# Kernel tuning notes

Hardware: AMD Instinct MI355X
Metric: run time of the kernel (lower is better)

Reference implementation:

```python
import jax, jax.numpy as jnp
import numpy as np

K = 11  # masked conv3d kernel size

def mask_A(k):
    # mask type 'A': flattened (i,j,t) positions with current_id < k^3//2 + 1
    # (current_id starts at 1) -> first k^3//2 positions are 1.
    m = (np.arange(k ** 3) < (k ** 3) // 2).astype(np.float32).reshape(k, k, k)
    return jnp.asarray(m)

def conv3d(x, w, b, pad):
    out = jax.lax.conv_general_dilated(
        x, w, window_strides=(1, 1, 1), padding=[(pad, pad)] * 3,
        dimension_numbers=('NCDHW', 'OIDHW', 'NCDHW'))
    return out + b[None, :, None, None, None]

def conv2d(x, w, b, pad):
    out = jax.lax.conv_general_dilated(
        x, w, window_strides=(1, 1), padding=[(pad, pad)] * 2,
        dimension_numbers=('NCHW', 'OIHW', 'NCHW'))
    return out + b[None, :, None, None]

def pconv(x, w, b):
    # 1x1x1 conv3d as channel GEMM; w: [O, C]
    return jnp.einsum('bcdhw,oc->bodhw', x, w) + b[None, :, None, None, None]

def _phi(z):
    return 0.5 * (1.0 + jax.lax.erf(z / jnp.sqrt(2.0).astype(z.dtype)))

def setup_inputs() -> dict:
    key = jax.random.key(0)
    ks = jax.random.split(key, 12)
    M = 192
    B, H, W = 1, 48, 48
    s = 0.02
    x = jax.random.normal(ks[0], (B, M, H, W), jnp.float32)
    hyper = jax.random.normal(ks[1], (B, 2 * M, H, W), jnp.float32)
    W3 = s * jax.random.normal(ks[2], (M, 2 * M, 3, 3), jnp.float32)
    b3 = jnp.zeros((M,), jnp.float32)
    W1 = s * jax.random.normal(ks[3], (24, 1, K, K, K), jnp.float32)
    b1 = jnp.zeros((24,), jnp.float32)
    Wa = s * jax.random.normal(ks[4], (48, 25), jnp.float32)
    ba = jnp.zeros((48,), jnp.float32)
    Wb = s * jax.random.normal(ks[5], (96, 48), jnp.float32)
    bb = jnp.zeros((96,), jnp.float32)
    Wc = s * jax.random.normal(ks[6], (9, 96), jnp.float32)
    bc = jnp.zeros((9,), jnp.float32)
    return {"x": x, "hyper": hyper, "W3": W3, "b3": b3, "W1": W1, "b1": b1,
            "Wa": Wa, "ba": ba, "Wb": Wb, "bb": bb, "Wc": Wc, "bc": bc}

def reference(x, hyper, W3, b3, W1, b1, Wa, ba, Wb, bb, Wc, bc):
    # x: [B,M,H,W], hyper: [B,2M,H,W]
    x5 = x[:, None]                                   # [B,1,M,H,W]
    h = conv2d(hyper, W3, b3, 1)[:, None]             # [B,1,M,H,W]
    W1m = W1 * mask_A(K)[None, None]                  # causal mask re-applied each fwd
    x1 = conv3d(x5, W1m, b1, 5)                       # [B,24,M,H,W]
    t = jnp.concatenate([x1, h], axis=1)              # [B,25,M,H,W]
    t = jax.nn.relu(pconv(t, Wa, ba))                 # [B,48,M,H,W]
    t = jax.nn.relu(pconv(t, Wb, bb))                 # [B,96,M,H,W]
    out = pconv(t, Wc, bc)                            # [B,9,M,H,W]
    # 3-component weighted Gaussian entropy model
    mu = out[:, 0:3]
    sc = out[:, 3:6]
    sc = jnp.abs(jnp.where(sc == 0.0, 1e-9, sc))
    w = jax.nn.softmax(out[:, 6:9], axis=1)
    xe = x[:, None]                                   # [B,1,M,H,W]
    lik = jnp.abs(_phi((xe + 0.5 - mu) / sc) - _phi((xe - 0.5 - mu) / sc))
    p3 = jnp.sum(w * lik, axis=1)                     # [B,M,H,W]
    return (p3, out)
```

## Files before the change

kernel.cpp:

```cpp
#include <hip/hip_runtime.h>
#include <hip/hip_fp16.h>
#include <math.h>

#define HW    2304
#define NPOS  442368

typedef _Float16 f16x8 __attribute__((ext_vector_type(8)));
typedef __fp16   h16x2 __attribute__((ext_vector_type(2)));
typedef float    f32x4 __attribute__((ext_vector_type(4)));

__device__ __forceinline__ float phi_f(float z) {
    return 0.5f * (1.0f + erff(z * 0.70710678118654752f));
}
__device__ __forceinline__ unsigned short f2h(float v) {
    _Float16 h = (_Float16)v;
    return *reinterpret_cast<unsigned short*>(&h);
}
__device__ __forceinline__ unsigned int pk2(float a, float b) {
    return (unsigned int)f2h(a) | ((unsigned int)f2h(b) << 16);
}
__device__ __forceinline__ unsigned int pkrtz(float a, float b) {
    h16x2 h = __builtin_amdgcn_cvt_pkrtz(a, b);
    return *reinterpret_cast<unsigned int*>(&h);
}

__global__ __launch_bounds__(256) void prep_all(const float* __restrict__ hyper,
                                                const float* __restrict__ W3,
                                                const float* __restrict__ W1,
                                                const float* __restrict__ Wa,
                                                const float* __restrict__ ba,
                                                const float* __restrict__ b1,
                                                const float* __restrict__ Wb,
                                                const float* __restrict__ bb,
                                                const float* __restrict__ Wc,
                                                const float* __restrict__ xg,
                                                unsigned short* __restrict__ hyperTp,
                                                unsigned short* __restrict__ apack,
                                                unsigned short* __restrict__ pk,
                                                unsigned short* __restrict__ xhp) {
    const int bx = blockIdx.x;
    if (bx < 948) {
        __shared__ float s[32][33];
        const int pt = bx % 79, it = bx / 79;
        const int tid = threadIdx.x;
        const int c = tid & 31, r = tid >> 5;
        const int pp = pt * 32 + c;
        const int yp = pp / 50, xp = pp % 50;
        const bool inter = (pp < 2500) && yp >= 1 && yp <= 48 && xp >= 1 && xp <= 48;
        const int src = inter ? ((yp - 1) * 48 + (xp - 1)) : 0;
#pragma unroll
        for (int i = 0; i < 4; ++i) {
            int icl = r + i * 8;
            s[icl][c] = inter ? hyper[(size_t)(it * 32 + icl) * HW + src] : 0.f;
        }
        __syncthreads();
#pragma unroll
        for (int i = 0; i < 4; ++i) {
            int pl = r + i * 8;
            int pp2 = pt * 32 + pl;
            if (pp2 < 2500)
                hyperTp[(size_t)pp2 * 384 + it * 32 + c] = f2h(s[c][pl]);
        }
    } else if (bx < 3540) {
        int idx = (bx - 948) * 256 + threadIdx.x;
        int j = idx & 7;
        int l = (idx >> 3) & 63;
        int rest = idx >> 9;
        int t = rest % 9; rest /= 9;
        int c = rest % 12; int T = rest / 12;
        int oc = T * 16 + (l & 15);
        int ic = c * 32 + (l >> 4) * 8 + j;
        apack[idx] = f2h(W3[((size_t)oc * 384 + ic) * 9 + t]);
    } else if (bx < 3700) {
        int idx = (bx - 3540) * 256 + threadIdx.x;
        if (idx >= 40960) return;
        float v = 0.f;
        if (idx < 31744) {
            int j = idx & 7, lane = (idx >> 3) & 63, s = (idx >> 9) & 1, c = idx >> 10;
            int q = lane >> 4;
            int oc = s * 16 + (lane & 15);
            int r = 2 * c + (q >> 1), h = q & 1, kw = 8 * h + j;
            if (oc < 24 && r < 61 && kw < 11) {
                int kd = r / 11, kh = r % 11;
                int tap = kd * 121 + kh * 11 + kw;
                if (tap < 665) v = W1[oc * 1331 + tap];
            }
        } else if (idx < 33280) {
            int i2 = idx - 31744;
            int j = i2 & 7, lane = (i2 >> 3) & 63, t = i2 >> 9;
            int m = t * 16 + (lane & 15), k = (lane >> 4) * 8 + j;
            if (k < 25) v = Wa[m * 25 + k];
            else if (k == 25) {
                float s = ba[m];
                for (int c = 0; c < 24; ++c) s += Wa[m * 25 + c] * b1[c];
                v = s;
            }
        } else if (idx < 39424) {
            int i3 = idx - 33280;
            int j = i3 & 7, lane = (i3 >> 3) & 63, k2 = (i3 >> 9) & 1, s = i3 >> 10;
            int m = s * 16 + (lane & 15), ch = k2 * 32 + (lane >> 4) * 8 + j;
            if (ch < 48) v = Wb[m * 48 + ch];
            else if (ch == 48) v = bb[m];
        } else {
            int i4 = idx - 39424;
            int j = i4 & 7, lane = (i4 >> 3) & 63, k3 = i4 >> 9;
            int m = lane & 15, ch = k3 * 32 + (lane >> 4) * 8 + j;
            if (m < 9) v = Wc[m * 96 + ch];
        }
        pk[idx] = f2h(v);
    } else {
        int idx = (bx - 3700) * 256 + threadIdx.x;
        if (idx >= 187456) return;
        int si = idx * 4;
        int zp = si / 3712, rem = si - zp * 3712;
        int yp = rem >> 6, xp0 = rem & 63;
        float f[4];
#pragma unroll
        for (int k = 0; k < 4; ++k) {
            int xp = xp0 + k;
            bool in = zp >= 5 && zp < 197 && yp >= 5 && yp < 53 && xp >= 5 && xp < 53;
            f[k] = in ? xg[(size_t)(zp - 5) * HW + (yp - 5) * 48 + (xp - 5)] : 0.f;
        }
        *(uint2*)&xhp[si] = make_uint2(pk2(f[0], f[1]), pk2(f[2], f[3]));
    }
}

__global__ __launch_bounds__(256) void fused3(const unsigned short* __restrict__ xhp,
                                              const unsigned short* __restrict__ pk,
                                              const unsigned short* __restrict__ hyperTp,
                                              const unsigned short* __restrict__ apack,
                                              const float* __restrict__ b3,
                                              const float* __restrict__ xg,
                                              const float* __restrict__ bc,
                                              float* __restrict__ out) {
    __shared__ __align__(16) unsigned short P[6656];
    __shared__ __align__(16) unsigned short t1s[4][1152];
    __shared__ __align__(16) unsigned short t2s[4][1664];
    __shared__ __align__(16) float fscr[3328];
    __shared__ __align__(16) float htile[256];

    const int tid = threadIdx.x, w = tid >> 6, lane = tid & 63;
    const int n = lane & 15, q = lane >> 4;
    const int bx = blockIdx.x;
    const int x0 = (bx % 12) * 4, y0 = ((bx / 12) % 12) * 4;
    const int T = bx / 144, d0 = T * 16;

#pragma unroll
    for (int k = 0; k < 3; ++k) {
        int idx = tid + k * 256;
        if (idx < 588) {
            int row = idx >> 1, half = idx & 1;
            int py = row / 21, pz = row - py * 21;
            const uint4* src = (const uint4*)(xhp + ((size_t)(d0 + pz) * 58 + (y0 + py)) * 64
                                              + x0 + half * 8);
            *(uint4*)&P[row * 16 + half * 8] = *src;
        }
    }

    {
        f32x4 hacc = {0.f, 0.f, 0.f, 0.f};
        const int pp = (y0 + (n >> 2)) * 50 + x0 + (n & 3);
        const size_t bbase = (size_t)pp * 384 + q * 8;
        for (int cc = 0; cc < 3; ++cc) {
            const int c = w * 3 + cc;
            const unsigned short* ap = apack + ((size_t)(T * 12 + c) * 9) * 512 + lane * 8;
            const int coff = c * 32;
#pragma unroll
            for (int t = 0; t < 9; ++t) {
                f16x8 a = *(const f16x8*)(ap + t * 512);
                const int dd = (t / 3) * 50 + (t % 3);
                f16x8 b = *(const f16x8*)(hyperTp + bbase + (size_t)dd * 384 + coff);
                hacc = __builtin_amdgcn_mfma_f32_16x16x32_f16(a, b, hacc, 0, 0, 0);
            }
        }
#pragma unroll
        for (int e = 0; e < 4; ++e)
            fscr[w * 256 + (q * 4 + e) * 16 + n] = hacc[e];
    }
    __syncthreads();

    {
        const int oc = tid >> 4, pos = tid & 15;
        float h = b3[d0 + oc];
#pragma unroll
        for (int ww = 0; ww < 4; ++ww) h += fscr[ww * 256 + oc * 16 + pos];
        htile[oc * 16 + pos] = h;
    }

    const f32x4 zf = {0.f, 0.f, 0.f, 0.f};
    f32x4 acc[4][2];
#pragma unroll
    for (int p = 0; p < 4; ++p) { acc[p][0] = zf; acc[p][1] = zf; }

    const f16x8* Av = (const f16x8*)pk;
    f16x8 a0 = Av[lane], a1 = Av[64 + lane];
    unsigned int u[6];
    {
        const int r0 = (q >> 1);
        const int kd = r0 / 11, kh = r0 - kd * 11;
        const unsigned short* rp = P + ((w + kh) * 21 + (n + kd)) * 16 + (q & 1) * 8;
        *(uint4*)&u[0] = *(const uint4*)rp;
        *(uint2*)&u[4] = *(const uint2*)(rp + 8);
    }
    for (int c = 0; c < 31; ++c) {
        unsigned int u2[6];
        {
            const int r = 2 * (c + 1) + (q >> 1);
            const int kd = r / 11, kh = r - kd * 11;
            const unsigned short* rp = P + ((w + kh) * 21 + (n + kd)) * 16 + (q & 1) * 8;
            *(uint4*)&u2[0] = *(const uint4*)rp;
            *(uint2*)&u2[4] = *(const uint2*)(rp + 8);
        }
        f16x8 ca0 = a0, ca1 = a1;
        const int cn = (c < 30) ? c + 1 : 30;
        a0 = Av[cn * 128 + lane];
        a1 = Av[cn * 128 + 64 + lane];
#pragma unroll
        for (int px = 0; px < 4; ++px) {
            unsigned int bw[4];
#pragma unroll
            for (int i = 0; i < 4; ++i) {
                if ((px & 1) == 0) bw[i] = u[(px >> 1) + i];
                else bw[i] = (u[(px >> 1) + i] >> 16) | (u[(px >> 1) + 1 + i] << 16);
            }
            f16x8 bf = *(f16x8*)bw;
            acc[px][0] = __builtin_amdgcn_mfma_f32_16x16x32_f16(ca0, bf, acc[px][0], 0, 0, 0);
            acc[px][1] = __builtin_amdgcn_mfma_f32_16x16x32_f16(ca1, bf, acc[px][1], 0, 0, 0);
        }
#pragma unroll
        for (int i = 0; i < 6; ++i) u[i] = u2[i];
    }
    __syncthreads();

#pragma unroll
    for (int px = 0; px < 4; ++px) {
        unsigned int lo = pk2(acc[px][0][0], acc[px][0][1]);
        unsigned int hi = pk2(acc[px][0][2], acc[px][0][3]);
        *(uint2*)&P[(w * 16 + n) * 104 + px * 24 + q * 4] = make_uint2(lo, hi);
        if (q < 2) {
            unsigned int l2 = pk2(acc[px][1][0], acc[px][1][1]);
            unsigned int h2 = pk2(acc[px][1][2], acc[px][1][3]);
            *(uint2*)&P[(w * 16 + n) * 104 + px * 24 + 16 + q * 4] = make_uint2(l2, h2);
        }
    }

    const volatile f16x8* WaF = (const volatile f16x8*)(pk + 31744);
    const volatile f16x8* WbF = (const volatile f16x8*)(pk + 33280);
    const volatile f16x8* WcF = (const volatile f16x8*)(pk + 39424);
    float bcv[4];
#pragma unroll
    for (int e = 0; e < 4; ++e) bcv[e] = (q * 4 + e < 9) ? bc[q * 4 + e] : 0.f;
    *(uint2*)&t1s[w][n * 72 + 48 + q * 4] = make_uint2((q == 0) ? 0x00003C00u : 0u, 0u);

    const f16x8 z8 = {};
    for (int px = 0; px < 4; ++px) {
        f16x8 b0;
        if (q < 3) {
            b0 = *(const f16x8*)&P[(w * 16 + n) * 104 + px * 24 + q * 8];
        } else {
            b0 = z8;
            b0[0] = (_Float16)htile[n * 16 + w * 4 + px];
            b0[1] = (_Float16)1.0f;
        }
#pragma unroll
        for (int s = 0; s < 3; ++s) {
            f16x8 a = WaF[s * 64 + lane];
            f32x4 r1 = __builtin_amdgcn_mfma_f32_16x16x32_f16(a, b0, zf, 0, 0, 0);
            *(uint2*)&t1s[w][n * 72 + s * 16 + q * 4] =
                make_uint2(pkrtz(fmaxf(r1[0], 0.f), fmaxf(r1[1], 0.f)),
                           pkrtz(fmaxf(r1[2], 0.f), fmaxf(r1[3], 0.f)));
        }
        f32x4 rb[6];
#pragma unroll
        for (int s = 0; s < 6; ++s) rb[s] = zf;
#pragma unroll
        for (int k2 = 0; k2 < 2; ++k2) {
            f16x8 bf = *(const f16x8*)&t1s[w][n * 72 + k2 * 32 + q * 8];
#pragma unroll
            for (int s = 0; s < 6; ++s) {
                f16x8 a = WbF[(s * 2 + k2) * 64 + lane];
                rb[s] = __builtin_amdgcn_mfma_f32_16x16x32_f16(a, bf, rb[s], 0, 0, 0);
            }
        }
#pragma unroll
        for (int s = 0; s < 6; ++s)
            *(uint2*)&t2s[w][n * 104 + s * 16 + q * 4] =
                make_uint2(pkrtz(fmaxf(rb[s][0], 0.f), fmaxf(rb[s][1], 0.f)),
                           pkrtz(fmaxf(rb[s][2], 0.f), fmaxf(rb[s][3], 0.f)));
        f32x4 rc = zf;
#pragma unroll
        for (int k3 = 0; k3 < 3; ++k3) {
            f16x8 bf = *(const f16x8*)&t2s[w][n * 104 + k3 * 32 + q * 8];
            f16x8 a = WcF[k3 * 64 + lane];
            rc = __builtin_amdgcn_mfma_f32_16x16x32_f16(a, bf, rc, 0, 0, 0);
        }
#pragma unroll
        for (int e = 0; e < 4; ++e) {
            const int row = q * 4 + e;
            if (row < 9) fscr[w * 832 + (n * 4 + px) * 13 + row] = rc[e] + bcv[e];
        }
    }

    {
        float o[9];
#pragma unroll
        for (int jj = 0; jj < 9; ++jj) o[jj] = fscr[w * 832 + lane * 13 + jj];
        const int gp = (d0 + (lane >> 2)) * HW + (y0 + w) * 48 + x0 + (lane & 3);
        const float xv = xg[gp];
        float m = fmaxf(o[6], fmaxf(o[7], o[8]));
        float e0 = expf(o[6] - m), e1 = expf(o[7] - m), e2 = expf(o[8] - m);
        float inv_es = 1.0f / (e0 + e1 + e2);
        float p = 0.f;
#pragma unroll
        for (int jj = 0; jj < 3; ++jj) {
            float mu = o[jj];
            float sc = o[3 + jj];
            sc = (sc == 0.0f) ? 1e-9f : sc;
            sc = fabsf(sc);
            float a = phi_f((xv + 0.5f - mu) / sc);
            float b = phi_f((xv - 0.5f - mu) / sc);
            float lik = fabsf(a - b);
            float wgt = ((jj == 0) ? e0 : (jj == 1) ? e1 : e2) * inv_es;
            p = fmaf(wgt, lik, p);
        }
        out[gp] = p;
#pragma unroll
        for (int jj = 0; jj < 9; ++jj) out[NPOS + (size_t)jj * NPOS + gp] = o[jj];
    }
}

extern "C" void kernel_launch(void* const* d_in, const int* in_sizes, int n_in,
                              void* d_out, int out_size, void* d_ws, size_t ws_size,
                              hipStream_t stream) {
    const float* x     = (const float*)d_in[0];
    const float* hyper = (const float*)d_in[1];
    const float* W3    = (const float*)d_in[2];
    const float* b3    = (const float*)d_in[3];
    const float* W1    = (const float*)d_in[4];
    const float* b1    = (const float*)d_in[5];
    const float* Wa    = (const float*)d_in[6];
    const float* ba    = (const float*)d_in[7];
    const float* Wb    = (const float*)d_in[8];
    const float* bb    = (const float*)d_in[9];
    const float* Wc    = (const float*)d_in[10];
    const float* bc    = (const float*)d_in[11];
    float* out = (float*)d_out;

    unsigned short* hyperTp = (unsigned short*)d_ws;
    unsigned short* apack   = hyperTp + 960000;
    unsigned short* pk      = apack + 663552;
    unsigned short* xhp     = pk + 40960;

    prep_all<<<4433, 256, 0, stream>>>(hyper, W3, W1, Wa, ba, b1, Wb, bb, Wc, x,
                                       hyperTp, apack, pk, xhp);
    fused3<<<1728, 256, 0, stream>>>(xhp, pk, hyperTp, apack, b3, x, bc, out);
}
```

Baseline: 182.5 us.

## Shrink fused3 LDS via buffer aliasing, hoist MLP weights, fully unroll conv loop

Merges the t1s, t2s and fscr shared buffers into one aliased region and reuses P for the final 9-channel outputs, which cuts LDS per block so more blocks can be resident. It sets launch_bounds(256,4) to target higher occupancy. The MLP weights are preloaded into registers instead of being reloaded through volatile pointers, and the 31-step masked conv loop is fully unrolled with compile-time offsets in place of the manual double-buffered prefetch. The risks are register pressure from the hoisted weights under the occupancy bound, and lost load/MFMA overlap if the compiler schedules the unrolled loop poorly.

```diff
diff --git a/kernel.cpp b/kernel.cpp
--- a/kernel.cpp
+++ b/kernel.cpp
@@ -125,18 +125,16 @@
     }
 }
 
-__global__ __launch_bounds__(256) void fused3(const unsigned short* __restrict__ xhp,
-                                              const unsigned short* __restrict__ pk,
-                                              const unsigned short* __restrict__ hyperTp,
-                                              const unsigned short* __restrict__ apack,
-                                              const float* __restrict__ b3,
-                                              const float* __restrict__ xg,
-                                              const float* __restrict__ bc,
-                                              float* __restrict__ out) {
+__global__ __launch_bounds__(256, 4) void fused3(const unsigned short* __restrict__ xhp,
+                                                 const unsigned short* __restrict__ pk,
+                                                 const unsigned short* __restrict__ hyperTp,
+                                                 const unsigned short* __restrict__ apack,
+                                                 const float* __restrict__ b3,
+                                                 const float* __restrict__ xg,
+                                                 const float* __restrict__ bc,
+                                                 float* __restrict__ out) {
     __shared__ __align__(16) unsigned short P[6656];
-    __shared__ __align__(16) unsigned short t1s[4][1152];
-    __shared__ __align__(16) unsigned short t2s[4][1664];
-    __shared__ __align__(16) float fscr[3328];
+    __shared__ __align__(16) unsigned short U[11264];
     __shared__ __align__(16) float htile[256];
 
     const int tid = threadIdx.x, w = tid >> 6, lane = tid & 63;
@@ -144,6 +142,8 @@
     const int bx = blockIdx.x;
     const int x0 = (bx % 12) * 4, y0 = ((bx / 12) % 12) * 4;
     const int T = bx / 144, d0 = T * 16;
+
+    float* hpart = (float*)U;
 
 #pragma unroll
     for (int k = 0; k < 3; ++k) {
@@ -161,6 +161,7 @@
         f32x4 hacc = {0.f, 0.f, 0.f, 0.f};
         const int pp = (y0 + (n >> 2)) * 50 + x0 + (n & 3);
         const size_t bbase = (size_t)pp * 384 + q * 8;
+#pragma unroll
         for (int cc = 0; cc < 3; ++cc) {
             const int c = w * 3 + cc;
             const unsigned short* ap = apack + ((size_t)(T * 12 + c) * 9) * 512 + lane * 8;
@@ -175,7 +176,7 @@
         }
 #pragma unroll
         for (int e = 0; e < 4; ++e)
-            fscr[w * 256 + (q * 4 + e) * 16 + n] = hacc[e];
+            hpart[w * 256 + (q * 4 + e) * 16 + n] = hacc[e];
     }
     __syncthreads();
 
@@ -183,7 +184,7 @@
         const int oc = tid >> 4, pos = tid & 15;
         float h = b3[d0 + oc];
 #pragma unroll
-        for (int ww = 0; ww < 4; ++ww) h += fscr[ww * 256 + oc * 16 + pos];
+        for (int ww = 0; ww < 4; ++ww) h += hpart[ww * 256 + oc * 16 + pos];
         htile[oc * 16 + pos] = h;
     }
 
@@ -193,28 +194,19 @@
     for (int p = 0; p < 4; ++p) { acc[p][0] = zf; acc[p][1] = zf; }
 
     const f16x8* Av = (const f16x8*)pk;
-    f16x8 a0 = Av[lane], a1 = Av[64 + lane];
-    unsigned int u[6];
-    {
-        const int r0 = (q >> 1);
-        const int kd = r0 / 11, kh = r0 - kd * 11;
-        const unsigned short* rp = P + ((w + kh) * 21 + (n + kd)) * 16 + (q & 1) * 8;
+    const int par = q >> 1;
+    const unsigned short* Pb = P + (w * 21 + n) * 16 + (q & 1) * 8;
+#pragma unroll
+    for (int c = 0; c < 31; ++c) {
+        const int r0 = 2 * c, r1 = 2 * c + 1;
+        const int o0 = ((r0 % 11) * 21 + (r0 / 11)) * 16;
+        const int o1 = ((r1 % 11) * 21 + (r1 / 11)) * 16;
+        const unsigned short* rp = Pb + (par ? o1 : o0);
+        unsigned int u[6];
         *(uint4*)&u[0] = *(const uint4*)rp;
         *(uint2*)&u[4] = *(const uint2*)(rp + 8);
-    }
-    for (int c = 0; c < 31; ++c) {
-        unsigned int u2[6];
-        {
-            const int r = 2 * (c + 1) + (q >> 1);
-            const int kd = r / 11, kh = r - kd * 11;
-            const unsigned short* rp = P + ((w + kh) * 21 + (n + kd)) * 16 + (q & 1) * 8;
-            *(uint4*)&u2[0] = *(const uint4*)rp;
-            *(uint2*)&u2[4] = *(const uint2*)(rp + 8);
-        }
-        f16x8 ca0 = a0, ca1 = a1;
-        const int cn = (c < 30) ? c + 1 : 30;
-        a0 = Av[cn * 128 + lane];
-        a1 = Av[cn * 128 + 64 + lane];
+        f16x8 ca0 = Av[c * 128 + lane];
+        f16x8 ca1 = Av[c * 128 + 64 + lane];
 #pragma unroll
         for (int px = 0; px < 4; ++px) {
             unsigned int bw[4];
@@ -227,8 +219,6 @@
             acc[px][0] = __builtin_amdgcn_mfma_f32_16x16x32_f16(ca0, bf, acc[px][0], 0, 0, 0);
             acc[px][1] = __builtin_amdgcn_mfma_f32_16x16x32_f16(ca1, bf, acc[px][1], 0, 0, 0);
         }
-#pragma unroll
-        for (int i = 0; i < 6; ++i) u[i] = u2[i];
     }
     __syncthreads();
 
@@ -244,13 +234,23 @@
         }
     }
 
-    const volatile f16x8* WaF = (const volatile f16x8*)(pk + 31744);
-    const volatile f16x8* WbF = (const volatile f16x8*)(pk + 33280);
-    const volatile f16x8* WcF = (const volatile f16x8*)(pk + 39424);
+    const f16x8* WaF = (const f16x8*)(pk + 31744);
+    const f16x8* WbF = (const f16x8*)(pk + 33280);
+    const f16x8* WcF = (const f16x8*)(pk + 39424);
+    f16x8 waf[3], wbf[12], wcf[3];
+#pragma unroll
+    for (int s = 0; s < 3; ++s) waf[s] = WaF[s * 64 + lane];
+#pragma unroll
+    for (int t = 0; t < 12; ++t) wbf[t] = WbF[t * 64 + lane];
+#pragma unroll
+    for (int k = 0; k < 3; ++k) wcf[k] = WcF[k * 64 + lane];
     float bcv[4];
 #pragma unroll
     for (int e = 0; e < 4; ++e) bcv[e] = (q * 4 + e < 9) ? bc[q * 4 + e] : 0.f;
-    *(uint2*)&t1s[w][n * 72 + 48 + q * 4] = make_uint2((q == 0) ? 0x00003C00u : 0u, 0u);
+
+    unsigned short* t1w = U + w * 1152;
+    unsigned short* t2w = U + 4608 + w * 1664;
+    *(uint2*)&t1w[n * 72 + 48 + q * 4] = make_uint2((q == 0) ? 0x00003C00u : 0u, 0u);
 
     const f16x8 z8 = {};
     for (int px = 0; px < 4; ++px) {
@@ -264,9 +264,8 @@
         }
 #pragma unroll
         for (int s = 0; s < 3; ++s) {
-            f16x8 a = WaF[s * 64 + lane];
-            f32x4 r1 = __builtin_amdgcn_mfma_f32_16x16x32_f16(a, b0, zf, 0, 0, 0);
-            *(uint2*)&t1s[w][n * 72 + s * 16 + q * 4] =
+            f32x4 r1 = __builtin_amdgcn_mfma_f32_16x16x32_f16(waf[s], b0, zf, 0, 0, 0);
+            *(uint2*)&t1w[n * 72 + s * 16 + q * 4] =
                 make_uint2(pkrtz(fmaxf(r1[0], 0.f), fmaxf(r1[1], 0.f)),
                            pkrtz(fmaxf(r1[2], 0.f), fmaxf(r1[3], 0.f)));
         }
@@ -275,46 +274,49 @@
         for (int s = 0; s < 6; ++s) rb[s] = zf;
 #pragma unroll
         for (int k2 = 0; k2 < 2; ++k2) {
-            f16x8 bf = *(const f16x8*)&t1s[w][n * 72 + k2 * 32 + q * 8];
-#pragma unroll
-            for (int s = 0; s < 6; ++s) {
-                f16x8 a = WbF[(s * 2 + k2) * 64 + lane];
-                rb[s] = __builtin_amdgcn_mfma_f32_16x16x32_f16(a, bf, rb[s], 0, 0, 0);
-            }
+            f16x8 bf = *(const f16x8*)&t1w[n * 72 + k2 * 32 + q * 8];
+#pragma unroll
+            for (int s = 0; s < 6; ++s)
+                rb[s] = __builtin_amdgcn_mfma_f32_16x16x32_f16(wbf[s * 2 + k2], bf, rb[s], 0, 0, 0);
         }
 #pragma unroll
         for (int s = 0; s < 6; ++s)
-            *(uint2*)&t2s[w][n * 104 + s * 16 + q * 4] =
+            *(uint2*)&t2w[n * 104 + s * 16 + q * 4] =
                 make_uint2(pkrtz(fmaxf(rb[s][0], 0.f), fmaxf(rb[s][1], 0.f)),
                            pkrtz(fmaxf(rb[s][2], 0.f), fmaxf(rb[s][3], 0.f)));
         f32x4 rc = zf;
 #pragma unroll
         for (int k3 = 0; k3 < 3; ++k3) {
-            f16x8 bf = *(const f16x8*)&t2s[w][n * 104 + k3 * 32 + q * 8];
-            f16x8 a = WcF[k3 * 64 + lane];
-            rc = __builtin_amdgcn_mfma_f32_16x16x32_f16(a, bf, rc, 0, 0, 0);
-        }
-#pragma unroll
-        for (int e = 0; e < 4; ++e) {
-            const int row = q * 4 + e;
-            if (row < 9) fscr[w * 832 + (n * 4 + px) * 13 + row] = rc[e] + bcv[e];
+            f16x8 bf = *(const f16x8*)&t2w[n * 104 + k3 * 32 + q * 8];
+            rc = __builtin_amdgcn_mfma_f32_16x16x32_f16(wcf[k3], bf, rc, 0, 0, 0);
+        }
+        {
+            float* pr = (float*)(P + (w * 16 + n) * 104 + px * 24);
+#pragma unroll
+            for (int e = 0; e < 4; ++e) {
+                const int row = q * 4 + e;
+                if (row < 9) pr[row] = rc[e] + bcv[e];
+            }
         }
     }
 
     {
-        float o[9];
-#pragma unroll
-        for (int jj = 0; jj < 9; ++jj) o[jj] = fscr[w * 832 + lane * 13 + jj];
+        const float* pr = (const float*)(P + (w * 16 + (lane >> 2)) * 104 + (lane & 3) * 24);
+        f32x4 oA = *(const f32x4*)pr;
+        f32x4 oB = *(const f32x4*)(pr + 4);
+        float o8 = pr[8];
         const int gp = (d0 + (lane >> 2)) * HW + (y0 + w) * 48 + x0 + (lane & 3);
         const float xv = xg[gp];
-        float m = fmaxf(o[6], fmaxf(o[7], o[8]));
-        float e0 = expf(o[6] - m), e1 = expf(o[7] - m), e2 = expf(o[8] - m);
+        float m = fmaxf(oB[2], fmaxf(oB[3], o8));
+        float e0 = expf(oB[2] - m), e1 = expf(oB[3] - m), e2 = expf(o8 - m);
         float inv_es = 1.0f / (e0 + e1 + e2);
+        float mu0 = oA[0], mu1 = oA[1], mu2 = oA[2];
+        float s0 = oA[3], s1 = oB[0], s2 = oB[1];
         float p = 0.f;
 #pragma unroll
         for (int jj = 0; jj < 3; ++jj) {
-            float mu = o[jj];
-            float sc = o[3 + jj];
+            float mu = (jj == 0) ? mu0 : (jj == 1) ? mu1 : mu2;
+            float sc = (jj == 0) ? s0 : (jj == 1) ? s1 : s2;
             sc = (sc == 0.0f) ? 1e-9f : sc;
             sc = fabsf(sc);
             float a = phi_f((xv + 0.5f - mu) / sc);
@@ -324,8 +326,15 @@
             p = fmaf(wgt, lik, p);
         }
         out[gp] = p;
-#pragma unroll
-        for (int jj = 0; jj < 9; ++jj) out[NPOS + (size_t)jj * NPOS + gp] = o[jj];
+        out[NPOS + (size_t)0 * NPOS + gp] = mu0;
+        out[NPOS + (size_t)1 * NPOS + gp] = mu1;
+        out[NPOS + (size_t)2 * NPOS + gp] = mu2;
+        out[NPOS + (size_t)3 * NPOS + gp] = s0;
+        out[NPOS + (size_t)4 * NPOS + gp] = s1;
+        out[NPOS + (size_t)5 * NPOS + gp] = s2;
+        out[NPOS + (size_t)6 * NPOS + gp] = oB[2];
+        out[NPOS + (size_t)7 * NPOS + gp] = oB[3];
+        out[NPOS + (size_t)8 * NPOS + gp] = o8;
     }
 }
 
```

Result: faster. 151.8 us (-16.8%).
